# Kernel optimization log

Hardware: AMD Instinct MI355X
Metric: run time of the kernel (lower is better)

Reference implementation:

```python
import jax, jax.numpy as jnp
import numpy as np

TOPO_SIZE = 128
TOPO_WEIGHT = 1.0


def setup_inputs() -> dict:
    key = jax.random.key(0)
    k1, k2 = jax.random.split(key)
    B, C, H, W = 16, 1, 1024, 1024
    labels = jax.random.randint(k1, (B, C, H, W), 0, 2).astype(jnp.float32)
    predictions = jax.random.normal(k2, (B, C, H, W), dtype=jnp.float32)
    return {"labels": labels, "predictions": predictions}


def _bce_with_logits_mean(logits, targets):
    # numerically stable BCE-with-logits, mean reduction (matches torch default)
    return jnp.mean(jnp.maximum(logits, 0.0) - logits * targets
                    + jnp.log1p(jnp.exp(-jnp.abs(logits))))


def _patchify(x, p):
    # x: [B, H, W] -> [B, nPatches, p*p]
    B, H, W = x.shape
    nH, nW = H // p, W // p
    x = x[:, :nH * p, :nW * p].reshape(B, nH, p, nW, p)
    return x.transpose(0, 1, 3, 2, 4).reshape(B, nH * nW, p * p)


def _topo_loss_per_sample(lh, gt, topo_size):
    # Surrogate for persistent-homology topo loss (external get_topo_loss):
    # crop into topo_size x topo_size patches; for patches whose ground truth
    # contains both classes (non-trivial topology), penalize the likelihood at
    # the patch's extremal critical points: (max(lh)-1)^2 + (min(lh)-0)^2.
    lh_p = _patchify(lh, topo_size)   # [B, P, p*p]
    gt_p = _patchify(gt, topo_size)   # [B, P, p*p]
    gmax = jnp.max(gt_p, axis=-1)
    gmin = jnp.min(gt_p, axis=-1)
    valid = (gmax > 0.5) & (gmin < 0.5)            # patch has both classes
    pmax = jnp.max(lh_p, axis=-1)
    pmin = jnp.min(lh_p, axis=-1)
    patch_loss = (pmax - 1.0) ** 2 + pmin ** 2
    return jnp.sum(jnp.where(valid, patch_loss, 0.0), axis=1)  # [B]


def reference(labels, predictions):
    bce = _bce_with_logits_mean(predictions, labels)
    # original flips both maps before the topo term
    inv_labels = 1.0 - labels
    inv_preds = 1.0 - predictions
    lh = jax.nn.sigmoid(inv_preds)[:, 0]   # squeeze channel -> [B, H, W]
    gt = inv_labels[:, 0]
    topo = jnp.mean(_topo_loss_per_sample(lh, gt, TOPO_SIZE))
    return bce + TOPO_WEIGHT * topo
```

## Files before the change

kernel.cpp:

```cpp
#include <hip/hip_runtime.h>
#include <math.h>

constexpr int B_ = 16;
constexpr int HW = 1024;
constexpr int P  = 128;
constexpr int NPATCH = 1024;
constexpr int THREADS1 = 512;

__global__ __launch_bounds__(THREADS1)
void patch_stats_kernel(const float* __restrict__ labels,
                        const float* __restrict__ preds,
                        float4* __restrict__ ws)
{
    const int pid = blockIdx.x;
    const int s  = pid >> 6;
    const int ph = (pid >> 3) & 7;
    const int pw = pid & 7;
    const size_t base = (size_t)s * (HW * HW) + (size_t)ph * P * HW + (size_t)pw * P;

    const int tid  = threadIdx.x;
    const int col4 = (tid & 31) << 2;
    const int row0 = tid >> 5;

    const float4* px = reinterpret_cast<const float4*>(preds  + base + (size_t)row0 * HW + col4);
    const float4* pt = reinterpret_cast<const float4*>(labels + base + (size_t)row0 * HW + col4);
    constexpr int STRIDE4 = 16 * HW / 4;

    float4 xb[8], tb[8];
    #pragma unroll
    for (int it = 0; it < 8; ++it) xb[it] = px[(size_t)it * STRIDE4];
    #pragma unroll
    for (int it = 0; it < 8; ++it) tb[it] = pt[(size_t)it * STRIDE4];

    float sum_relu = 0.0f, sum_xt = 0.0f, sum_l2 = 0.0f;
    float xmin =  3.0e38f, xmax = -3.0e38f;
    float tmin =  3.0e38f, tmax = -3.0e38f;

    const float NLOG2E = -1.4426950408889634f;

    #pragma unroll
    for (int it = 0; it < 8; ++it) {
        const float xs[4] = {xb[it].x, xb[it].y, xb[it].z, xb[it].w};
        const float ts[4] = {tb[it].x, tb[it].y, tb[it].z, tb[it].w};
        #pragma unroll
        for (int j = 0; j < 4; ++j) {
            const float x = xs[j], t = ts[j];
            const float e = __builtin_amdgcn_exp2f(fabsf(x) * NLOG2E);
            sum_l2   += __builtin_amdgcn_logf(1.0f + e);
            sum_relu += fmaxf(x, 0.0f);
            sum_xt    = fmaf(x, t, sum_xt);
            xmin = fminf(xmin, x); xmax = fmaxf(xmax, x);
            tmin = fminf(tmin, t); tmax = fmaxf(tmax, t);
        }
    }

    const float LN2 = 0.6931471805599453f;
    float bce = sum_relu - sum_xt + LN2 * sum_l2;

    #pragma unroll
    for (int o = 32; o > 0; o >>= 1) {
        bce += __shfl_down(bce, o);
        xmin = fminf(xmin, __shfl_down(xmin, o));
        xmax = fmaxf(xmax, __shfl_down(xmax, o));
        tmin = fminf(tmin, __shfl_down(tmin, o));
        tmax = fmaxf(tmax, __shfl_down(tmax, o));
    }

    __shared__ float s_bce[8], s_xmin[8], s_xmax[8], s_tmin[8], s_tmax[8];
    const int wave = tid >> 6;
    const int lane = tid & 63;
    if (lane == 0) {
        s_bce[wave] = bce;  s_xmin[wave] = xmin; s_xmax[wave] = xmax;
        s_tmin[wave] = tmin; s_tmax[wave] = tmax;
    }
    __syncthreads();
    if (tid == 0) {
        float b = 0.0f, xi = 3.0e38f, xa = -3.0e38f, ti = 3.0e38f, ta = -3.0e38f;
        #pragma unroll
        for (int w = 0; w < THREADS1 / 64; ++w) {
            b += s_bce[w];
            xi = fminf(xi, s_xmin[w]); xa = fmaxf(xa, s_xmax[w]);
            ti = fminf(ti, s_tmin[w]); ta = fmaxf(ta, s_tmax[w]);
        }
        const float valid = (ti < 0.5f && ta > 0.5f) ? 1.0f : 0.0f;
        ws[pid] = make_float4(b, xi, xa, valid);
    }
}

__global__ __launch_bounds__(256)
void final_reduce_kernel(const float4* __restrict__ ws, float* __restrict__ out)
{
    const int tid = threadIdx.x;
    float bce = 0.0f, topo = 0.0f;
    for (int i = tid; i < NPATCH; i += 256) {
        const float4 rec = ws[i];
        bce += rec.x;
        if (rec.w > 0.5f) {
            const float pmax = 1.0f / (1.0f + __expf(rec.y - 1.0f));
            const float pmin = 1.0f / (1.0f + __expf(rec.z - 1.0f));
            topo += (pmax - 1.0f) * (pmax - 1.0f) + pmin * pmin;
        }
    }
    #pragma unroll
    for (int o = 32; o > 0; o >>= 1) {
        bce  += __shfl_down(bce, o);
        topo += __shfl_down(topo, o);
    }
    __shared__ float s_b[4], s_t[4];
    const int wave = tid >> 6;
    const int lane = tid & 63;
    if (lane == 0) { s_b[wave] = bce; s_t[wave] = topo; }
    __syncthreads();
    if (tid == 0) {
        const float bt = s_b[0] + s_b[1] + s_b[2] + s_b[3];
        const float tt = s_t[0] + s_t[1] + s_t[2] + s_t[3];
        out[0] = bt / (float)((size_t)B_ * HW * HW) + tt / (float)B_;
    }
}

extern "C" void kernel_launch(void* const* d_in, const int* in_sizes, int n_in,
                              void* d_out, int out_size, void* d_ws, size_t ws_size,
                              hipStream_t stream) {
    const float* labels = (const float*)d_in[0];
    const float* preds  = (const float*)d_in[1];
    float*  out = (float*)d_out;
    float4* ws  = (float4*)d_ws;

    patch_stats_kernel<<<NPATCH, THREADS1, 0, stream>>>(labels, preds, ws);
    final_reduce_kernel<<<1, 256, 0, stream>>>(ws, out);
}
```

Before: 31.25 us.

## Fuse final reduction into patch kernel via last-block atomic ticket

Merges the two kernels into one: each block writes its patch record, fences, and takes an atomic ticket, and the last block to finish performs the global reduction and writes the output. It also interleaves the prediction and label loads and adds a scheduling barrier so all loads are issued before compute. This removes a second kernel launch and its gap, but adds a memset launch to reset the counter and a serial tail in the last block.

```diff
diff --git a/kernel.cpp b/kernel.cpp
--- a/kernel.cpp
+++ b/kernel.cpp
@@ -8,9 +8,11 @@
 constexpr int THREADS1 = 512;
 
 __global__ __launch_bounds__(THREADS1)
-void patch_stats_kernel(const float* __restrict__ labels,
-                        const float* __restrict__ preds,
-                        float4* __restrict__ ws)
+void fused_loss_kernel(const float* __restrict__ labels,
+                       const float* __restrict__ preds,
+                       float4* __restrict__ recs,
+                       unsigned int* __restrict__ counter,
+                       float* __restrict__ out)
 {
     const int pid = blockIdx.x;
     const int s  = pid >> 6;
@@ -28,9 +30,11 @@
 
     float4 xb[8], tb[8];
     #pragma unroll
-    for (int it = 0; it < 8; ++it) xb[it] = px[(size_t)it * STRIDE4];
-    #pragma unroll
-    for (int it = 0; it < 8; ++it) tb[it] = pt[(size_t)it * STRIDE4];
+    for (int it = 0; it < 8; ++it) {
+        xb[it] = px[(size_t)it * STRIDE4];
+        tb[it] = pt[(size_t)it * STRIDE4];
+    }
+    __builtin_amdgcn_sched_barrier(0);
 
     float sum_relu = 0.0f, sum_xt = 0.0f, sum_l2 = 0.0f;
     float xmin =  3.0e38f, xmax = -3.0e38f;
@@ -66,55 +70,56 @@
         tmax = fmaxf(tmax, __shfl_down(tmax, o));
     }
 
-    __shared__ float s_bce[8], s_xmin[8], s_xmax[8], s_tmin[8], s_tmax[8];
+    __shared__ float s_a[8], s_b2[8], s_c[8], s_d[8], s_e[8];
+    __shared__ unsigned int s_ticket;
     const int wave = tid >> 6;
     const int lane = tid & 63;
     if (lane == 0) {
-        s_bce[wave] = bce;  s_xmin[wave] = xmin; s_xmax[wave] = xmax;
-        s_tmin[wave] = tmin; s_tmax[wave] = tmax;
+        s_a[wave] = bce;  s_b2[wave] = xmin; s_c[wave] = xmax;
+        s_d[wave] = tmin; s_e[wave] = tmax;
     }
     __syncthreads();
     if (tid == 0) {
         float b = 0.0f, xi = 3.0e38f, xa = -3.0e38f, ti = 3.0e38f, ta = -3.0e38f;
         #pragma unroll
         for (int w = 0; w < THREADS1 / 64; ++w) {
-            b += s_bce[w];
-            xi = fminf(xi, s_xmin[w]); xa = fmaxf(xa, s_xmax[w]);
-            ti = fminf(ti, s_tmin[w]); ta = fmaxf(ta, s_tmax[w]);
+            b += s_a[w];
+            xi = fminf(xi, s_b2[w]); xa = fmaxf(xa, s_c[w]);
+            ti = fminf(ti, s_d[w]); ta = fmaxf(ta, s_e[w]);
         }
         const float valid = (ti < 0.5f && ta > 0.5f) ? 1.0f : 0.0f;
-        ws[pid] = make_float4(b, xi, xa, valid);
+        recs[pid] = make_float4(b, xi, xa, valid);
+        __threadfence();
+        s_ticket = atomicAdd(counter, 1u);
     }
-}
+    __syncthreads();
 
-__global__ __launch_bounds__(256)
-void final_reduce_kernel(const float4* __restrict__ ws, float* __restrict__ out)
-{
-    const int tid = threadIdx.x;
-    float bce = 0.0f, topo = 0.0f;
-    for (int i = tid; i < NPATCH; i += 256) {
-        const float4 rec = ws[i];
-        bce += rec.x;
-        if (rec.w > 0.5f) {
-            const float pmax = 1.0f / (1.0f + __expf(rec.y - 1.0f));
-            const float pmin = 1.0f / (1.0f + __expf(rec.z - 1.0f));
-            topo += (pmax - 1.0f) * (pmax - 1.0f) + pmin * pmin;
+    if (s_ticket == NPATCH - 1) {
+        __threadfence();
+        float bsum = 0.0f, topo = 0.0f;
+        for (int i = tid; i < NPATCH; i += THREADS1) {
+            const float4 rec = recs[i];
+            bsum += rec.x;
+            if (rec.w > 0.5f) {
+                const float pmax = 1.0f / (1.0f + __expf(rec.y - 1.0f));
+                const float pmin = 1.0f / (1.0f + __expf(rec.z - 1.0f));
+                topo += (pmax - 1.0f) * (pmax - 1.0f) + pmin * pmin;
+            }
         }
-    }
-    #pragma unroll
-    for (int o = 32; o > 0; o >>= 1) {
-        bce  += __shfl_down(bce, o);
-        topo += __shfl_down(topo, o);
-    }
-    __shared__ float s_b[4], s_t[4];
-    const int wave = tid >> 6;
-    const int lane = tid & 63;
-    if (lane == 0) { s_b[wave] = bce; s_t[wave] = topo; }
-    __syncthreads();
-    if (tid == 0) {
-        const float bt = s_b[0] + s_b[1] + s_b[2] + s_b[3];
-        const float tt = s_t[0] + s_t[1] + s_t[2] + s_t[3];
-        out[0] = bt / (float)((size_t)B_ * HW * HW) + tt / (float)B_;
+        #pragma unroll
+        for (int o = 32; o > 0; o >>= 1) {
+            bsum += __shfl_down(bsum, o);
+            topo += __shfl_down(topo, o);
+        }
+        __syncthreads();
+        if (lane == 0) { s_a[wave] = bsum; s_b2[wave] = topo; }
+        __syncthreads();
+        if (tid == 0) {
+            float bt = 0.0f, tt = 0.0f;
+            #pragma unroll
+            for (int w = 0; w < THREADS1 / 64; ++w) { bt += s_a[w]; tt += s_b2[w]; }
+            out[0] = bt / (float)((size_t)B_ * HW * HW) + tt / (float)B_;
+        }
     }
 }
 
@@ -124,8 +129,9 @@
     const float* labels = (const float*)d_in[0];
     const float* preds  = (const float*)d_in[1];
     float*  out = (float*)d_out;
-    float4* ws  = (float4*)d_ws;
+    float4* recs = (float4*)d_ws;
+    unsigned int* counter = (unsigned int*)((char*)d_ws + NPATCH * sizeof(float4));
 
-    patch_stats_kernel<<<NPATCH, THREADS1, 0, stream>>>(labels, preds, ws);
-    final_reduce_kernel<<<1, 256, 0, stream>>>(ws, out);
+    hipMemsetAsync(counter, 0, sizeof(unsigned int), stream);
+    fused_loss_kernel<<<NPATCH, THREADS1, 0, stream>>>(labels, preds, recs, counter, out);
 }
```

Result: slower. 64.53 us (+106.5%).

## Stream contiguous row bands through LDS with triple-buffered async global loads

Applied to the files above, without the earlier changes.

Each block now covers a contiguous 32-row band and reads it in wave-contiguous 1 KB chunks, instead of one 128x128 patch read with row-strided accesses. The chunks go straight to LDS through global_load_lds and a three-slot ring with manual vmcnt waits, so loads overlap with the compute. Per-quarter-patch partials (sum, min/max) are written out and combined per patch in a larger final reduce kernel. This adds LDS traffic, more workspace records and a bigger second kernel in exchange for sequential access and latency hiding.

```diff
diff --git a/kernel.cpp b/kernel.cpp
--- a/kernel.cpp
+++ b/kernel.cpp
@@ -3,117 +3,135 @@
 
 constexpr int B_ = 16;
 constexpr int HW = 1024;
-constexpr int P  = 128;
 constexpr int NPATCH = 1024;
-constexpr int THREADS1 = 512;
+constexpr int NQ = 512;
+constexpr int T1 = 512;
 
-__global__ __launch_bounds__(THREADS1)
-void patch_stats_kernel(const float* __restrict__ labels,
-                        const float* __restrict__ preds,
-                        float4* __restrict__ ws)
+typedef __attribute__((address_space(3))) unsigned int lds_uint;
+typedef __attribute__((address_space(1))) const unsigned int glob_uint;
+
+__device__ __forceinline__ void gload16(const float* g, char* lds_generic) {
+    __builtin_amdgcn_global_load_lds((glob_uint*)g, (lds_uint*)lds_generic, 16, 0, 0);
+}
+
+__global__ __launch_bounds__(T1)
+void stream_kernel(const float* __restrict__ labels,
+                   const float* __restrict__ preds,
+                   float4* __restrict__ recs)
 {
-    const int pid = blockIdx.x;
-    const int s  = pid >> 6;
-    const int ph = (pid >> 3) & 7;
-    const int pw = pid & 7;
-    const size_t base = (size_t)s * (HW * HW) + (size_t)ph * P * HW + (size_t)pw * P;
+    __shared__ __align__(16) char smem[8 * 3 * 2048];
+    __shared__ float parts[8][2][5];
 
-    const int tid  = threadIdx.x;
-    const int col4 = (tid & 31) << 2;
-    const int row0 = tid >> 5;
+    const int qid = blockIdx.x;
+    const int tid = threadIdx.x;
+    const int w = tid >> 6, l = tid & 63;
 
-    const float4* px = reinterpret_cast<const float4*>(preds  + base + (size_t)row0 * HW + col4);
-    const float4* pt = reinterpret_cast<const float4*>(labels + base + (size_t)row0 * HW + col4);
-    constexpr int STRIDE4 = 16 * HW / 4;
+    const size_t qbase = (size_t)qid * (32 * HW);
+    const int lane_off = w * 256 + l * 4;
+    const float* gx = preds  + qbase + lane_off;
+    const float* gt = labels + qbase + lane_off;
+    char* wslot = smem + w * (3 * 2048);
 
-    float4 xb[8], tb[8];
     #pragma unroll
-    for (int it = 0; it < 8; ++it) xb[it] = px[(size_t)it * STRIDE4];
-    #pragma unroll
-    for (int it = 0; it < 8; ++it) tb[it] = pt[(size_t)it * STRIDE4];
+    for (int c = 0; c < 2; ++c) {
+        gload16(gx + c * 2048, wslot + (c % 3) * 2048);
+        gload16(gt + c * 2048, wslot + (c % 3) * 2048 + 1024);
+    }
 
-    float sum_relu = 0.0f, sum_xt = 0.0f, sum_l2 = 0.0f;
-    float xmin =  3.0e38f, xmax = -3.0e38f;
-    float tmin =  3.0e38f, tmax = -3.0e38f;
-
+    float sum_relu = 0.f, sum_xt = 0.f, sum_l2 = 0.f;
+    float xmin = 3.0e38f, xmax = -3.0e38f, tmin = 3.0e38f, tmax = -3.0e38f;
     const float NLOG2E = -1.4426950408889634f;
 
     #pragma unroll
-    for (int it = 0; it < 8; ++it) {
-        const float xs[4] = {xb[it].x, xb[it].y, xb[it].z, xb[it].w};
-        const float ts[4] = {tb[it].x, tb[it].y, tb[it].z, tb[it].w};
+    for (int c = 0; c < 16; ++c) {
+        if (c + 2 < 16) {
+            gload16(gx + (c + 2) * 2048, wslot + ((c + 2) % 3) * 2048);
+            gload16(gt + (c + 2) * 2048, wslot + ((c + 2) % 3) * 2048 + 1024);
+        }
+        if (c < 14)       { asm volatile("s_waitcnt vmcnt(4)" ::: "memory"); }
+        else if (c == 14) { asm volatile("s_waitcnt vmcnt(2)" ::: "memory"); }
+        else              { asm volatile("s_waitcnt vmcnt(0)" ::: "memory"); }
+        __builtin_amdgcn_sched_barrier(0);
+
+        const char* xs = wslot + (c % 3) * 2048 + l * 16;
+        const float4 x4 = *reinterpret_cast<const float4*>(xs);
+        const float4 t4 = *reinterpret_cast<const float4*>(xs + 1024);
+        const float xv[4] = {x4.x, x4.y, x4.z, x4.w};
+        const float tv[4] = {t4.x, t4.y, t4.z, t4.w};
         #pragma unroll
         for (int j = 0; j < 4; ++j) {
-            const float x = xs[j], t = ts[j];
+            const float x = xv[j], t = tv[j];
             const float e = __builtin_amdgcn_exp2f(fabsf(x) * NLOG2E);
             sum_l2   += __builtin_amdgcn_logf(1.0f + e);
-            sum_relu += fmaxf(x, 0.0f);
+            sum_relu += fmaxf(x, 0.f);
             sum_xt    = fmaf(x, t, sum_xt);
             xmin = fminf(xmin, x); xmax = fmaxf(xmax, x);
             tmin = fminf(tmin, t); tmax = fmaxf(tmax, t);
         }
     }
-
-    const float LN2 = 0.6931471805599453f;
-    float bce = sum_relu - sum_xt + LN2 * sum_l2;
+    float bce = sum_relu - sum_xt + 0.6931471805599453f * sum_l2;
 
     #pragma unroll
-    for (int o = 32; o > 0; o >>= 1) {
-        bce += __shfl_down(bce, o);
-        xmin = fminf(xmin, __shfl_down(xmin, o));
-        xmax = fmaxf(xmax, __shfl_down(xmax, o));
-        tmin = fminf(tmin, __shfl_down(tmin, o));
-        tmax = fmaxf(tmax, __shfl_down(tmax, o));
+    for (int o = 16; o > 0; o >>= 1) {
+        bce += __shfl_down(bce, o, 32);
+        xmin = fminf(xmin, __shfl_down(xmin, o, 32));
+        xmax = fmaxf(xmax, __shfl_down(xmax, o, 32));
+        tmin = fminf(tmin, __shfl_down(tmin, o, 32));
+        tmax = fmaxf(tmax, __shfl_down(tmax, o, 32));
     }
-
-    __shared__ float s_bce[8], s_xmin[8], s_xmax[8], s_tmin[8], s_tmax[8];
-    const int wave = tid >> 6;
-    const int lane = tid & 63;
-    if (lane == 0) {
-        s_bce[wave] = bce;  s_xmin[wave] = xmin; s_xmax[wave] = xmax;
-        s_tmin[wave] = tmin; s_tmax[wave] = tmax;
+    if ((l & 31) == 0) {
+        const int p = 2 * (w & 3) + (l >> 5);
+        const int j = w >> 2;
+        parts[p][j][0] = bce;  parts[p][j][1] = xmin; parts[p][j][2] = xmax;
+        parts[p][j][3] = tmin; parts[p][j][4] = tmax;
     }
     __syncthreads();
-    if (tid == 0) {
-        float b = 0.0f, xi = 3.0e38f, xa = -3.0e38f, ti = 3.0e38f, ta = -3.0e38f;
-        #pragma unroll
-        for (int w = 0; w < THREADS1 / 64; ++w) {
-            b += s_bce[w];
-            xi = fminf(xi, s_xmin[w]); xa = fmaxf(xa, s_xmax[w]);
-            ti = fminf(ti, s_tmin[w]); ta = fmaxf(ta, s_tmax[w]);
-        }
-        const float valid = (ti < 0.5f && ta > 0.5f) ? 1.0f : 0.0f;
-        ws[pid] = make_float4(b, xi, xa, valid);
+    if (tid < 8) {
+        const int p = tid;
+        const float b  = parts[p][0][0] + parts[p][1][0];
+        const float xi = fminf(parts[p][0][1], parts[p][1][1]);
+        const float xa = fmaxf(parts[p][0][2], parts[p][1][2]);
+        const float ti = fminf(parts[p][0][3], parts[p][1][3]);
+        const float ta = fmaxf(parts[p][0][4], parts[p][1][4]);
+        const int s = qid >> 5, q = qid & 31, pb = q >> 2, qq = q & 3;
+        const int idx = ((s * 64 + pb * 8 + p) * 4 + qq) * 2;
+        recs[idx]     = make_float4(b, xi, xa, 0.f);
+        recs[idx + 1] = make_float4(ti, ta, 0.f, 0.f);
     }
 }
 
-__global__ __launch_bounds__(256)
-void final_reduce_kernel(const float4* __restrict__ ws, float* __restrict__ out)
+__global__ __launch_bounds__(1024)
+void final_reduce_kernel(const float4* __restrict__ recs, float* __restrict__ out)
 {
-    const int tid = threadIdx.x;
-    float bce = 0.0f, topo = 0.0f;
-    for (int i = tid; i < NPATCH; i += 256) {
-        const float4 rec = ws[i];
-        bce += rec.x;
-        if (rec.w > 0.5f) {
-            const float pmax = 1.0f / (1.0f + __expf(rec.y - 1.0f));
-            const float pmin = 1.0f / (1.0f + __expf(rec.z - 1.0f));
-            topo += (pmax - 1.0f) * (pmax - 1.0f) + pmin * pmin;
-        }
+    const int t = threadIdx.x;
+    float b = 0.f, xi = 3.0e38f, xa = -3.0e38f, ti = 3.0e38f, ta = -3.0e38f;
+    #pragma unroll
+    for (int qq = 0; qq < 4; ++qq) {
+        const float4 rA = recs[(t * 4 + qq) * 2];
+        const float4 rB = recs[(t * 4 + qq) * 2 + 1];
+        b += rA.x;
+        xi = fminf(xi, rA.y); xa = fmaxf(xa, rA.z);
+        ti = fminf(ti, rB.x); ta = fmaxf(ta, rB.y);
+    }
+    float topo = 0.f;
+    if (ti < 0.5f && ta > 0.5f) {
+        const float pmax = 1.0f / (1.0f + __expf(xi - 1.0f));
+        const float pmin = 1.0f / (1.0f + __expf(xa - 1.0f));
+        topo = (pmax - 1.f) * (pmax - 1.f) + pmin * pmin;
     }
     #pragma unroll
     for (int o = 32; o > 0; o >>= 1) {
-        bce  += __shfl_down(bce, o);
+        b += __shfl_down(b, o);
         topo += __shfl_down(topo, o);
     }
-    __shared__ float s_b[4], s_t[4];
-    const int wave = tid >> 6;
-    const int lane = tid & 63;
-    if (lane == 0) { s_b[wave] = bce; s_t[wave] = topo; }
+    __shared__ float sb[16], st[16];
+    const int wv = t >> 6, ln = t & 63;
+    if (ln == 0) { sb[wv] = b; st[wv] = topo; }
     __syncthreads();
-    if (tid == 0) {
-        const float bt = s_b[0] + s_b[1] + s_b[2] + s_b[3];
-        const float tt = s_t[0] + s_t[1] + s_t[2] + s_t[3];
+    if (t == 0) {
+        float bt = 0.f, tt = 0.f;
+        #pragma unroll
+        for (int i = 0; i < 16; ++i) { bt += sb[i]; tt += st[i]; }
         out[0] = bt / (float)((size_t)B_ * HW * HW) + tt / (float)B_;
     }
 }
@@ -123,9 +141,9 @@
                               hipStream_t stream) {
     const float* labels = (const float*)d_in[0];
     const float* preds  = (const float*)d_in[1];
-    float*  out = (float*)d_out;
-    float4* ws  = (float4*)d_ws;
+    float*  out  = (float*)d_out;
+    float4* recs = (float4*)d_ws;
 
-    patch_stats_kernel<<<NPATCH, THREADS1, 0, stream>>>(labels, preds, ws);
-    final_reduce_kernel<<<1, 256, 0, stream>>>(ws, out);
+    stream_kernel<<<NQ, T1, 0, stream>>>(labels, preds, recs);
+    final_reduce_kernel<<<1, 1024, 0, stream>>>(recs, out);
 }
```

New measurement: 32.71 us. 1.05x slower.
